# Optimization experiments

Hardware: AMD Instinct MI355X
Metric: run time of the kernel (lower is better)

## Reference

```python
import jax, jax.numpy as jnp
import numpy as np
from math import sqrt, pi

EMBED, HEADS, ATTN, MLP = 1024, 16, 1024, 4096
HEAD_DIM = ATTN // HEADS
EPS = 1e-5

def _ln(x):
    mu = jnp.mean(x, axis=-1, keepdims=True)
    var = jnp.var(x, axis=-1, keepdims=True)
    return (x - mu) / jnp.sqrt(var + EPS)

def _gelu(x):
    return 0.5 * x * (1.0 + jnp.tanh(sqrt(2.0 / pi) * (x + 0.044715 * x**3)))

def setup_inputs() -> dict:
    key = jax.random.key(0)
    ks = jax.random.split(key, 6)
    B, S = 2, 2048
    x = jax.random.normal(ks[0], (B, S, EMBED), dtype=jnp.float32)
    # weights stored as [in, out] (transpose of torch's [out, in]); math identical
    w_qkv = jax.random.normal(ks[1], (EMBED, 3 * ATTN), dtype=jnp.float32) / sqrt(EMBED)
    w_fc = jax.random.normal(ks[2], (ATTN, EMBED), dtype=jnp.float32) / sqrt(ATTN)
    w1 = jax.random.normal(ks[3], (EMBED, MLP), dtype=jnp.float32) / sqrt(EMBED)
    b1 = jnp.zeros((MLP,), dtype=jnp.float32)
    w2 = jax.random.normal(ks[4], (MLP, EMBED), dtype=jnp.float32) / sqrt(MLP)
    b2 = jnp.zeros((EMBED,), dtype=jnp.float32)
    return {"x": x, "w_qkv": w_qkv, "w_fc": w_fc, "w1": w1, "b1": b1, "w2": w2, "b2": b2}

def reference(x, w_qkv, w_fc, w1, b1, w2, b2):
    B, S, _ = x.shape
    res = x
    h = _ln(x)
    qkv = h @ w_qkv                                   # [B,S,3*ATTN]
    q, k, v = jnp.split(qkv, 3, axis=-1)
    q = q.reshape(B, S, HEADS, HEAD_DIM)
    k = k.reshape(B, S, HEADS, HEAD_DIM)
    v = v.reshape(B, S, HEADS, HEAD_DIM)
    attn = jnp.einsum('bqnc,bknc->bnqk', q, k) / sqrt(HEAD_DIM)  # [B,H,S,S]
    attn = jax.nn.softmax(attn, axis=-1)
    attn_val = jnp.einsum('bnqk,bknc->bqnc', attn, v).reshape(B, S, ATTN)
    x = res + attn_val @ w_fc
    res = x
    h = _ln(x)
    h = _gelu(h @ w1 + b1) @ w2 + b2
    return res + h
```

## Files before the change

### kernel.cpp

```cpp
#include <hip/hip_runtime.h>

typedef unsigned short u16;
typedef __attribute__((ext_vector_type(8))) short bf16x8;
typedef __attribute__((ext_vector_type(4))) short s16x4;
typedef __attribute__((ext_vector_type(4))) float f32x4;

#define DEV __device__ __forceinline__

DEV u16 f2bf(float f) {
  union { float f; unsigned u; } v; v.f = f;
  unsigned r = v.u + 0x7fffu + ((v.u >> 16) & 1u);
  return (u16)(r >> 16);
}
DEV u16 f2bf_tr(float f) {
  union { float f; unsigned u; } v; v.f = f;
  return (u16)(v.u >> 16);
}

DEV int swzi(int row, int col) { return row * 64 + (col ^ ((row & 7) << 3)); }

DEV void gl16(const u16* g, u16* l) {
  __builtin_amdgcn_global_load_lds((const __attribute__((address_space(1))) void*)g,
                                   (__attribute__((address_space(3))) void*)l, 16, 0, 0);
}

template <int N> DEV void waitv() {
  asm volatile("s_waitcnt vmcnt(%0)" :: "n"(N) : "memory");
}
DEV void barrier_f() {
  __builtin_amdgcn_s_barrier();
  asm volatile("" ::: "memory");
}
DEV void lgkm0() { asm volatile("s_waitcnt lgkmcnt(0)" ::: "memory"); }

__global__ __launch_bounds__(256) void wcastT(const float* __restrict__ w,
                                              u16* __restrict__ wt, int K, int N) {
  __shared__ float t[32][33];
  int n0 = blockIdx.x * 32, k0 = blockIdx.y * 32;
  int tx = threadIdx.x & 31, ty = threadIdx.x >> 5;
#pragma unroll
  for (int i = 0; i < 32; i += 8)
    t[ty + i][tx] = w[(size_t)(k0 + ty + i) * N + n0 + tx];
  __syncthreads();
#pragma unroll
  for (int i = 0; i < 32; i += 8)
    wt[(size_t)(n0 + ty + i) * K + k0 + tx] = f2bf(t[tx][ty + i]);
}

__global__ __launch_bounds__(256) void ln_kernel(const float* __restrict__ x,
                                                 u16* __restrict__ out) {
  int row = blockIdx.x, tid = threadIdx.x;
  const float4* xr = (const float4*)(x + (size_t)row * 1024);
  float4 f = xr[tid];
  float s = f.x + f.y + f.z + f.w;
  float s2 = f.x * f.x + f.y * f.y + f.z * f.z + f.w * f.w;
#pragma unroll
  for (int o = 1; o < 64; o <<= 1) { s += __shfl_xor(s, o); s2 += __shfl_xor(s2, o); }
  __shared__ float red[2][4];
  int wid = tid >> 6;
  if ((tid & 63) == 0) { red[0][wid] = s; red[1][wid] = s2; }
  __syncthreads();
  float tot  = red[0][0] + red[0][1] + red[0][2] + red[0][3];
  float tot2 = red[1][0] + red[1][1] + red[1][2] + red[1][3];
  float mu = tot * (1.0f / 1024.0f);
  float var = tot2 * (1.0f / 1024.0f) - mu * mu;
  float rstd = rsqrtf(var + 1e-5f);
  s16x4 o4;
  o4[0] = (short)f2bf((f.x - mu) * rstd);
  o4[1] = (short)f2bf((f.y - mu) * rstd);
  o4[2] = (short)f2bf((f.z - mu) * rstd);
  o4[3] = (short)f2bf((f.w - mu) * rstd);
  *(s16x4*)(out + (size_t)row * 1024 + tid * 4) = o4;
}

template <int MODE, int BM, int BK>
__global__ __launch_bounds__(256) void gemm_bt(
    const u16* __restrict__ A, const u16* __restrict__ Bt, int N, int K,
    const float* __restrict__ resid, const float* __restrict__ bias,
    float* __restrict__ outF, u16* __restrict__ o0, u16* __restrict__ o1,
    u16* __restrict__ o2) {
  constexpr int MR = BM / 32;
  constexpr int KH = BK / 32;
  constexpr int LDEPTH = KH * (BM / 64 + 2);
  constexpr int ACH = BM * 32, BCH = 128 * 32;
  __shared__ __align__(16) u16 lA[2 * KH * ACH];
  __shared__ __align__(16) u16 lB[2 * KH * BCH];
  int tid = threadIdx.x;
  int lane = tid & 63, wid = tid >> 6;
  int lr = lane & 15, lg = lane >> 4;

  int gx = gridDim.x;
  int nwg = gx * gridDim.y;
  int bid = blockIdx.y * gx + blockIdx.x;
  int swz = (bid & 7) * (nwg >> 3) + (bid >> 3);
  int rowBase = (swz / gx) * BM, colBase = (swz % gx) * 128;
  int wr = (wid >> 1) * (MR * 16), wc = (wid & 1) * 64;

  int srow = wid * 16 + (lane >> 2);
  int scol = (lane & 3) * 8;
  const u16* gA = A + (size_t)(rowBase + srow) * K + scol;
  const u16* gB = Bt + (size_t)(colBase + srow) * K + scol;
  u16* lAb = &lA[wid * 16 * 32];
  u16* lBb = &lB[wid * 16 * 32];

  auto stage = [&](int t, int buf) {
    int k0 = t * BK;
#pragma unroll
    for (int kk = 0; kk < KH; kk++) {
      u16* dA = lAb + buf * KH * ACH + kk * ACH;
      u16* dB = lBb + buf * KH * BCH + kk * BCH;
      int koff = k0 + kk * 32;
#pragma unroll
      for (int c = 0; c < BM / 64; c++)
        gl16(gA + (size_t)c * 64 * K + koff, dA + c * 64 * 32);
#pragma unroll
      for (int c = 0; c < 2; c++)
        gl16(gB + (size_t)c * 64 * K + koff, dB + c * 64 * 32);
    }
  };

  f32x4 acc[MR][4];
  f32x4 zero = {0.f, 0.f, 0.f, 0.f};
#pragma unroll
  for (int m = 0; m < MR; m++)
#pragma unroll
    for (int n = 0; n < 4; n++) acc[m][n] = zero;

  stage(0, 0);

  int nt = K / BK;
  for (int t = 0; t < nt; t++) {
    int cur = t & 1;
    if (t + 1 < nt) {
      stage(t + 1, cur ^ 1);
      waitv<LDEPTH>();
    } else {
      waitv<0>();
    }
    barrier_f();

    const u16* cA = &lA[cur * KH * ACH];
    const u16* cB = &lB[cur * KH * BCH];
#pragma unroll
    for (int kk = 0; kk < KH; kk++) {
      bf16x8 af[MR], bfv[4];
#pragma unroll
      for (int m = 0; m < MR; m++)
        af[m] = *(const bf16x8*)&cA[kk * ACH + (wr + m * 16 + lr) * 32 + lg * 8];
#pragma unroll
      for (int n = 0; n < 4; n++)
        bfv[n] = *(const bf16x8*)&cB[kk * BCH + (wc + n * 16 + lr) * 32 + lg * 8];
#pragma unroll
      for (int m = 0; m < MR; m++)
#pragma unroll
        for (int n = 0; n < 4; n++)
          acc[m][n] = __builtin_amdgcn_mfma_f32_16x16x32_bf16(bfv[n], af[m], acc[m][n], 0, 0, 0);
    }
    barrier_f();
  }

#pragma unroll
  for (int m = 0; m < MR; m++) {
    int grow = rowBase + wr + m * 16 + lr;
#pragma unroll
    for (int n = 0; n < 4; n++) {
      int gcol = colBase + wc + n * 16 + lg * 4;
      f32x4 v4 = acc[m][n];
      if constexpr (MODE == 0) {
        if (gcol < 2048) {
          bool isq = gcol < 1024;
          u16* dst = isq ? o0 : o1;
          s16x4 o4;
#pragma unroll
          for (int j = 0; j < 4; j++)
            o4[j] = (short)f2bf(isq ? v4[j] * 0.18033688011112042f : v4[j]);
          *(s16x4*)&dst[(size_t)grow * 1024 + (gcol & 1023)] = o4;
        } else {
          int c = gcol - 2048;
          int bb = grow >> 11, ss = grow & 2047;
          size_t vbase = ((size_t)bb * 1024 + c) * 2048 + ss;
#pragma unroll
          for (int j = 0; j < 4; j++)
            o2[vbase + (size_t)j * 2048] = f2bf(v4[j]);
        }
      } else if constexpr (MODE == 1) {
        size_t idx = (size_t)grow * N + gcol;
        float4 r = *(const float4*)&resid[idx];
        float4 ov = {r.x + v4[0], r.y + v4[1], r.z + v4[2], r.w + v4[3]};
        *(float4*)&outF[idx] = ov;
      } else {
        size_t idx = (size_t)grow * N + gcol;
        float4 r = *(const float4*)&resid[idx];
        float4 bq = *(const float4*)&bias[gcol];
        float4 ov = {r.x + bq.x + v4[0], r.y + bq.y + v4[1],
                     r.z + bq.z + v4[2], r.w + bq.w + v4[3]};
        *(float4*)&outF[idx] = ov;
      }
    }
  }
}

__global__ __launch_bounds__(512, 1) void gemm256p(
    const u16* __restrict__ A, const u16* __restrict__ Bt,
    const float* __restrict__ bias, u16* __restrict__ o0) {
  constexpr int K = 1024, N = 4096, NT = 16;
  __shared__ __align__(16) u16 lA[2 * 2 * 256 * 32];
  __shared__ __align__(16) u16 lB[2 * 2 * 256 * 32];
  int tid = threadIdx.x;
  int lane = tid & 63, wid = tid >> 6;
  int lr = lane & 15, lg = lane >> 4;
  int wm = wid >> 2, wn = wid & 3;

  int gx = gridDim.x;
  int nwg = gx * gridDim.y;
  int bid = blockIdx.y * gx + blockIdx.x;
  int swz = (bid & 7) * (nwg >> 3) + (bid >> 3);
  int rowBase = (swz / gx) * 256, colBase = (swz % gx) * 256;

  int sr0 = tid >> 2, sc = (tid & 3) * 8;
  const u16* gA = A + (size_t)(rowBase + sr0) * K + sc;
  const u16* gB = Bt + (size_t)(colBase + sr0) * K + sc;
  u16* lAw = lA + wid * 512;
  u16* lBw = lB + wid * 512;

  auto stageA = [&](int t, int kh) {
    int koff = t * 64 + kh * 32;
    u16* d = lAw + ((t & 1) * 2 + kh) * 8192;
    gl16(gA + koff, d);
    gl16(gA + (size_t)128 * K + koff, d + 4096);
  };
  auto stageB = [&](int t, int kh) {
    int koff = t * 64 + kh * 32;
    u16* d = lBw + ((t & 1) * 2 + kh) * 8192;
    gl16(gB + koff, d);
    gl16(gB + (size_t)128 * K + koff, d + 4096);
  };

  f32x4 acc[8][4];
  f32x4 zero = {0.f, 0.f, 0.f, 0.f};
#pragma unroll
  for (int m = 0; m < 8; m++)
#pragma unroll
    for (int n = 0; n < 4; n++) acc[m][n] = zero;

  bf16x8 aF[4][2], bF0[2][2], bF1[2][2];

  auto rdA = [&](int t, int rh) {
#pragma unroll
    for (int kh = 0; kh < 2; kh++) {
      const u16* p = lA + ((t & 1) * 2 + kh) * 8192;
#pragma unroll
      for (int m = 0; m < 4; m++)
        aF[m][kh] = *(const bf16x8*)&p[(wm * 128 + rh * 64 + m * 16 + lr) * 32 + lg * 8];
    }
  };
  auto rdB = [&](bf16x8 (&bb)[2][2], int t, int ch) {
#pragma unroll
    for (int kh = 0; kh < 2; kh++) {
      const u16* p = lB + ((t & 1) * 2 + kh) * 8192;
#pragma unroll
      for (int n = 0; n < 2; n++)
        bb[n][kh] = *(const bf16x8*)&p[(wn * 64 + ch * 32 + n * 16 + lr) * 32 + lg * 8];
    }
  };

  stageA(0, 0); stageA(0, 1); stageB(0, 0); stageB(0, 1);
  waitv<2>();
  barrier_f();

  for (int t = 0; t < NT; t++) {
    bool st = (t + 1 < NT);
    rdA(t, 0); rdB(bF0, t, 0);
    if (st) { stageA(t + 1, 0); stageA(t + 1, 1); }
    barrier_f(); lgkm0();
    __builtin_amdgcn_s_setprio(1);
#pragma unroll
    for (int m = 0; m < 4; m++)
#pragma unroll
      for (int n = 0; n < 2; n++)
#pragma unroll
        for (int kh = 0; kh < 2; kh++)
          acc[m][n] = __builtin_amdgcn_mfma_f32_16x16x32_bf16(bF0[n][kh], aF[m][kh], acc[m][n], 0, 0, 0);
    __builtin_amdgcn_s_setprio(0);
    if (st) waitv<4>(); else waitv<0>();
    barrier_f();
    rdB(bF1, t, 1);
    if (st) stageB(t + 1, 0);
    barrier_f(); lgkm0();
    __builtin_amdgcn_s_setprio(1);
#pragma unroll
    for (int m = 0; m < 4; m++)
#pragma unroll
      for (int n = 0; n < 2; n++)
#pragma unroll
        for (int kh = 0; kh < 2; kh++)
          acc[m][2 + n] = __builtin_amdgcn_mfma_f32_16x16x32_bf16(bF1[n][kh], aF[m][kh], acc[m][2 + n], 0, 0, 0);
    __builtin_amdgcn_s_setprio(0);
    barrier_f();
    rdA(t, 1);
    if (st) stageB(t + 1, 1);
    barrier_f(); lgkm0();
    __builtin_amdgcn_s_setprio(1);
#pragma unroll
    for (int m = 0; m < 4; m++)
#pragma unroll
      for (int n = 0; n < 2; n++)
#pragma unroll
        for (int kh = 0; kh < 2; kh++)
          acc[4 + m][n] = __builtin_amdgcn_mfma_f32_16x16x32_bf16(bF0[n][kh], aF[m][kh], acc[4 + m][n], 0, 0, 0);
    __builtin_amdgcn_s_setprio(0);
    barrier_f();
    barrier_f(); lgkm0();
    __builtin_amdgcn_s_setprio(1);
#pragma unroll
    for (int m = 0; m < 4; m++)
#pragma unroll
      for (int n = 0; n < 2; n++)
#pragma unroll
        for (int kh = 0; kh < 2; kh++)
          acc[4 + m][2 + n] = __builtin_amdgcn_mfma_f32_16x16x32_bf16(bF1[n][kh], aF[m][kh], acc[4 + m][2 + n], 0, 0, 0);
    __builtin_amdgcn_s_setprio(0);
    if (st) waitv<2>();
    barrier_f();
  }

#pragma unroll
  for (int mi = 0; mi < 8; mi++) {
    int grow = rowBase + wm * 128 + mi * 16 + lr;
#pragma unroll
    for (int ni = 0; ni < 4; ni++) {
      int gcol = colBase + wn * 64 + ni * 16 + lg * 4;
      f32x4 v4 = acc[mi][ni];
      float4 bq = *(const float4*)&bias[gcol];
      s16x4 o4;
#pragma unroll
      for (int j = 0; j < 4; j++) {
        float g = v4[j] + ((const float*)&bq)[j];
        float e = __builtin_amdgcn_exp2f(2.302208198f * (g + 0.044715f * g * g * g));
        o4[j] = (short)f2bf(g - g * __builtin_amdgcn_rcpf(1.0f + e));
      }
      *(s16x4*)&o0[(size_t)grow * N + gcol] = o4;
    }
  }
}

__global__ __launch_bounds__(256) void attn_kernel(const u16* __restrict__ q,
                                                   const u16* __restrict__ k,
                                                   const u16* __restrict__ vt,
                                                   u16* __restrict__ o) {
  __shared__ __align__(16) u16 lK[64 * 64];
  __shared__ __align__(16) u16 lV[64 * 64];
  __shared__ __align__(16) u16 lP[4 * 2 * 16 * 64];
  const int S = 2048, E = 1024;
  int qt = blockIdx.x, h = blockIdx.y, b = blockIdx.z;
  int tid = threadIdx.x, wid = tid >> 6, lane = tid & 63;
  int lr = lane & 15, lg = lane >> 4;
  u16* lPw = &lP[wid * 2048];

  const u16* qp = q + ((size_t)b * S + qt * 128 + wid * 32) * E + h * 64;
  const u16* kp = k + (size_t)b * S * E + h * 64;
  const u16* vp = vt + ((size_t)(b * 16 + h) * 64) * S;

  bf16x8 aQ[2][2];
#pragma unroll
  for (int m = 0; m < 2; m++)
#pragma unroll
    for (int kk = 0; kk < 2; kk++)
      aQ[m][kk] = *(const bf16x8*)(qp + (size_t)(m * 16 + lr) * E + kk * 32 + lg * 8);

  bf16x8 onesv;
#pragma unroll
  for (int i = 0; i < 8; i++) onesv[i] = (short)0x3F80;

  f32x4 accO[2][4], accL[2];
  f32x4 zero = {0.f, 0.f, 0.f, 0.f};
#pragma unroll
  for (int m = 0; m < 2; m++) {
    accL[m] = zero;
#pragma unroll
    for (int nn = 0; nn < 4; nn++) accO[m][nn] = zero;
  }

  int sr_ = tid >> 3, sc_ = (tid & 7) * 8;
  const u16* kps0 = kp + (size_t)sr_ * E + sc_;
  const u16* kps1 = kp + (size_t)(sr_ + 32) * E + sc_;
  const u16* vps0 = vp + (size_t)sr_ * S + sc_;
  const u16* vps1 = vp + (size_t)(sr_ + 32) * S + sc_;

  bf16x8 rk0 = *(const bf16x8*)(kps0);
  bf16x8 rk1 = *(const bf16x8*)(kps1);
  bf16x8 rv0 = *(const bf16x8*)(vps0);
  bf16x8 rv1 = *(const bf16x8*)(vps1);

  for (int kv0 = 0; kv0 < S; kv0 += 64) {
    __syncthreads();
    *(bf16x8*)&lK[swzi(sr_, sc_)] = rk0;
    *(bf16x8*)&lK[swzi(32 + sr_, sc_)] = rk1;
    *(bf16x8*)&lV[swzi(sr_, sc_)] = rv0;
    *(bf16x8*)&lV[swzi(32 + sr_, sc_)] = rv1;
    int nx = kv0 + 64;
    if (nx < S) {
      rk0 = *(const bf16x8*)(kps0 + (size_t)nx * E);
      rk1 = *(const bf16x8*)(kps1 + (size_t)nx * E);
      rv0 = *(const bf16x8*)(vps0 + nx);
      rv1 = *(const bf16x8*)(vps1 + nx);
    }
    __syncthreads();

    f32x4 sc4[2][4];
#pragma unroll
    for (int m = 0; m < 2; m++)
#pragma unroll
      for (int n = 0; n < 4; n++) sc4[m][n] = zero;
#pragma unroll
    for (int n = 0; n < 4; n++) {
      bf16x8 bk0 = *(const bf16x8*)&lK[swzi(n * 16 + lr, lg * 8)];
      bf16x8 bk1 = *(const bf16x8*)&lK[swzi(n * 16 + lr, 32 + lg * 8)];
#pragma unroll
      for (int m = 0; m < 2; m++) {
        sc4[m][n] = __builtin_amdgcn_mfma_f32_16x16x32_bf16(bk0, aQ[m][0], sc4[m][n], 0, 0, 0);
        sc4[m][n] = __builtin_amdgcn_mfma_f32_16x16x32_bf16(bk1, aQ[m][1], sc4[m][n], 0, 0, 0);
      }
    }

#pragma unroll
    for (int m = 0; m < 2; m++)
#pragma unroll
      for (int n = 0; n < 4; n++) {
        s16x4 pq;
#pragma unroll
        for (int j = 0; j < 4; j++)
          pq[j] = (short)f2bf_tr(__builtin_amdgcn_exp2f(sc4[m][n][j]));
        *(s16x4*)&lPw[m * 1024 + swzi(lr, n * 16 + lg * 4)] = pq;
      }

#pragma unroll
    for (int kk = 0; kk < 2; kk++) {
      bf16x8 ap[2];
#pragma unroll
      for (int m = 0; m < 2; m++)
        ap[m] = *(const bf16x8*)&lPw[m * 1024 + swzi(lr, kk * 32 + lg * 8)];
#pragma unroll
      for (int m = 0; m < 2; m++)
        accL[m] = __builtin_amdgcn_mfma_f32_16x16x32_bf16(onesv, ap[m], accL[m], 0, 0, 0);
#pragma unroll
      for (int nn = 0; nn < 4; nn++) {
        bf16x8 bv = *(const bf16x8*)&lV[swzi(nn * 16 + lr, kk * 32 + lg * 8)];
#pragma unroll
        for (int m = 0; m < 2; m++)
          accO[m][nn] = __builtin_amdgcn_mfma_f32_16x16x32_bf16(bv, ap[m], accO[m][nn], 0, 0, 0);
      }
    }
  }

#pragma unroll
  for (int m = 0; m < 2; m++) {
    float inv = 1.0f / accL[m][0];
    int srow = qt * 128 + wid * 32 + m * 16 + lr;
#pragma unroll
    for (int nn = 0; nn < 4; nn++) {
      s16x4 o4;
#pragma unroll
      for (int j = 0; j < 4; j++) o4[j] = (short)f2bf(accO[m][nn][j] * inv);
      *(s16x4*)&o[((size_t)b * S + srow) * E + h * 64 + nn * 16 + lg * 4] = o4;
    }
  }
}

extern "C" void kernel_launch(void* const* d_in, const int* in_sizes, int n_in,
                              void* d_out, int out_size, void* d_ws, size_t ws_size,
                              hipStream_t stream) {
  (void)in_sizes; (void)n_in; (void)out_size; (void)ws_size;
  const float* x     = (const float*)d_in[0];
  const float* w_qkv = (const float*)d_in[1];
  const float* w_fc  = (const float*)d_in[2];
  const float* w1    = (const float*)d_in[3];
  const float* b1    = (const float*)d_in[4];
  const float* w2    = (const float*)d_in[5];
  const float* b2    = (const float*)d_in[6];
  float* out = (float*)d_out;
  char* ws = (char*)d_ws;

  u16* wqkvT = (u16*)(ws);
  u16* wfcT  = (u16*)(ws + 6291456);
  u16* w1T   = (u16*)(ws + 8388608);
  u16* w2T   = (u16*)(ws + 16777216);
  u16* hbuf  = (u16*)(ws + 25165824);
  u16* qbuf  = (u16*)(ws + 33554432);
  u16* kbuf  = (u16*)(ws + 41943040);
  u16* vtbuf = (u16*)(ws + 58720256);
  float* x2  = (float*)(ws + 67108864);
  u16* act   = qbuf;

  wcastT<<<dim3(96, 32), 256, 0, stream>>>(w_qkv, wqkvT, 1024, 3072);
  wcastT<<<dim3(32, 32), 256, 0, stream>>>(w_fc, wfcT, 1024, 1024);
  wcastT<<<dim3(128, 32), 256, 0, stream>>>(w1, w1T, 1024, 4096);
  wcastT<<<dim3(32, 128), 256, 0, stream>>>(w2, w2T, 4096, 1024);

  ln_kernel<<<4096, 256, 0, stream>>>(x, hbuf);
  gemm_bt<0, 128, 32><<<dim3(24, 32), 256, 0, stream>>>(hbuf, wqkvT, 3072, 1024,
                                                        nullptr, nullptr, nullptr,
                                                        qbuf, kbuf, vtbuf);
  attn_kernel<<<dim3(16, 16, 2), 256, 0, stream>>>(qbuf, kbuf, vtbuf, hbuf);
  gemm_bt<1, 64, 64><<<dim3(8, 64), 256, 0, stream>>>(hbuf, wfcT, 1024, 1024,
                                                      x, nullptr, x2,
                                                      nullptr, nullptr, nullptr);
  ln_kernel<<<4096, 256, 0, stream>>>(x2, hbuf);
  gemm256p<<<dim3(16, 16), 512, 0, stream>>>(hbuf, w1T, b1, act);
  gemm_bt<3, 64, 64><<<dim3(8, 64), 256, 0, stream>>>(act, w2T, 1024, 4096,
                                                      x2, b2, out,
                                                      nullptr, nullptr, nullptr);
}
```

Baseline: 235.7 us.

## Collapse four-phase MFMA loop into two phases with full B fragment reads

Restructures the GEMM main loop so each K-tile reads all four B column fragments at once and runs two larger MFMA phases instead of four quarter phases. B staging for the next tile is issued together in the second phase, and the loop waits for all outstanding global-to-LDS loads at the end of each iteration. This cuts barriers and phase overhead per iteration. In exchange it uses more registers for B fragments and gives up finer-grained overlap of staging loads with compute.

Measured after the change: 239.4 us. About the same (+1.6%).

```diff
diff --git a/kernel.cpp b/kernel.cpp
--- a/kernel.cpp
+++ b/kernel.cpp
@@ -243,7 +243,7 @@
 #pragma unroll
     for (int n = 0; n < 4; n++) acc[m][n] = zero;
 
-  bf16x8 aF[4][2], bF0[2][2], bF1[2][2];
+  bf16x8 aF[4][2], bF[4][2];
 
   auto rdA = [&](int t, int rh) {
 #pragma unroll
@@ -254,73 +254,48 @@
         aF[m][kh] = *(const bf16x8*)&p[(wm * 128 + rh * 64 + m * 16 + lr) * 32 + lg * 8];
     }
   };
-  auto rdB = [&](bf16x8 (&bb)[2][2], int t, int ch) {
+  auto rdB = [&](int t) {
 #pragma unroll
     for (int kh = 0; kh < 2; kh++) {
       const u16* p = lB + ((t & 1) * 2 + kh) * 8192;
 #pragma unroll
-      for (int n = 0; n < 2; n++)
-        bb[n][kh] = *(const bf16x8*)&p[(wn * 64 + ch * 32 + n * 16 + lr) * 32 + lg * 8];
+      for (int n = 0; n < 4; n++)
+        bF[n][kh] = *(const bf16x8*)&p[(wn * 64 + n * 16 + lr) * 32 + lg * 8];
     }
   };
 
   stageA(0, 0); stageA(0, 1); stageB(0, 0); stageB(0, 1);
-  waitv<2>();
+  waitv<0>();
   barrier_f();
 
   for (int t = 0; t < NT; t++) {
     bool st = (t + 1 < NT);
-    rdA(t, 0); rdB(bF0, t, 0);
+    rdA(t, 0); rdB(t);
     if (st) { stageA(t + 1, 0); stageA(t + 1, 1); }
     barrier_f(); lgkm0();
     __builtin_amdgcn_s_setprio(1);
 #pragma unroll
     for (int m = 0; m < 4; m++)
 #pragma unroll
-      for (int n = 0; n < 2; n++)
+      for (int n = 0; n < 4; n++)
 #pragma unroll
         for (int kh = 0; kh < 2; kh++)
-          acc[m][n] = __builtin_amdgcn_mfma_f32_16x16x32_bf16(bF0[n][kh], aF[m][kh], acc[m][n], 0, 0, 0);
-    __builtin_amdgcn_s_setprio(0);
-    if (st) waitv<4>(); else waitv<0>();
-    barrier_f();
-    rdB(bF1, t, 1);
-    if (st) stageB(t + 1, 0);
-    barrier_f(); lgkm0();
-    __builtin_amdgcn_s_setprio(1);
-#pragma unroll
-    for (int m = 0; m < 4; m++)
-#pragma unroll
-      for (int n = 0; n < 2; n++)
-#pragma unroll
-        for (int kh = 0; kh < 2; kh++)
-          acc[m][2 + n] = __builtin_amdgcn_mfma_f32_16x16x32_bf16(bF1[n][kh], aF[m][kh], acc[m][2 + n], 0, 0, 0);
+          acc[m][n] = __builtin_amdgcn_mfma_f32_16x16x32_bf16(bF[n][kh], aF[m][kh], acc[m][n], 0, 0, 0);
     __builtin_amdgcn_s_setprio(0);
     barrier_f();
     rdA(t, 1);
-    if (st) stageB(t + 1, 1);
+    if (st) { stageB(t + 1, 0); stageB(t + 1, 1); }
     barrier_f(); lgkm0();
     __builtin_amdgcn_s_setprio(1);
 #pragma unroll
     for (int m = 0; m < 4; m++)
 #pragma unroll
-      for (int n = 0; n < 2; n++)
+      for (int n = 0; n < 4; n++)
 #pragma unroll
         for (int kh = 0; kh < 2; kh++)
-          acc[4 + m][n] = __builtin_amdgcn_mfma_f32_16x16x32_bf16(bF0[n][kh], aF[m][kh], acc[4 + m][n], 0, 0, 0);
+          acc[4 + m][n] = __builtin_amdgcn_mfma_f32_16x16x32_bf16(bF[n][kh], aF[m][kh], acc[4 + m][n], 0, 0, 0);
     __builtin_amdgcn_s_setprio(0);
-    barrier_f();
-    barrier_f(); lgkm0();
-    __builtin_amdgcn_s_setprio(1);
-#pragma unroll
-    for (int m = 0; m < 4; m++)
-#pragma unroll
-      for (int n = 0; n < 2; n++)
-#pragma unroll
-        for (int kh = 0; kh < 2; kh++)
-          acc[4 + m][2 + n] = __builtin_amdgcn_mfma_f32_16x16x32_bf16(bF1[n][kh], aF[m][kh], acc[4 + m][2 + n], 0, 0, 0);
-    __builtin_amdgcn_s_setprio(0);
-    if (st) waitv<2>();
+    waitv<0>();
     barrier_f();
   }
 
```
